# Kernel optimization log

Measured on AMD Instinct MI355X. Metric: run time of the kernel, lower is better.

## Reference

```python
import jax, jax.numpy as jnp
import numpy as np

K = 3          # kernel size
PAD = 1        # padding
KK = K * K
RECURRENT = 3  # opt.Recurrent_times - 1


def dcnv2(x, offset, mask, weight, bias):
    """Modulated deformable conv (DCNv2), stride 1, pad 1, dilation 1.

    x:      [B, C, H, W]
    offset: [B, 2*KK, H, W]  -- (dy, dx) interleaved per kernel tap
    mask:   [B, KK, H, W]    -- modulation scalars
    weight: [O, C, K, K], bias: [O]
    """
    B, C, H, W = x.shape
    off = offset.reshape(B, KK, 2, H, W)
    dy, dx = off[:, :, 0], off[:, :, 1]                       # [B,KK,H,W]

    ky, kx = jnp.meshgrid(jnp.arange(K), jnp.arange(K), indexing='ij')
    ky = (ky.reshape(KK) - PAD).astype(x.dtype)               # {-1,0,1}
    kx = (kx.reshape(KK) - PAD).astype(x.dtype)
    iy = jnp.arange(H, dtype=x.dtype)
    ix = jnp.arange(W, dtype=x.dtype)

    # fractional sampling coords, [B,KK,H,W]
    py = iy[None, None, :, None] + ky[None, :, None, None] + dy
    px = ix[None, None, None, :] + kx[None, :, None, None] + dx

    y0 = jnp.floor(py)
    x0 = jnp.floor(px)
    wy = (py - y0)[:, None]                                   # [B,1,KK,H,W]
    wx = (px - x0)[:, None]

    x_flat = x.reshape(B, C, H * W)

    def gather(yi, xi):
        valid = ((yi >= 0) & (yi <= H - 1) & (xi >= 0) & (xi <= W - 1))
        yc = jnp.clip(yi, 0, H - 1).astype(jnp.int32)
        xc = jnp.clip(xi, 0, W - 1).astype(jnp.int32)
        idx = (yc * W + xc).reshape(B, -1)                    # [B, KK*H*W]
        g = jax.vmap(lambda im, id_: im[:, id_])(x_flat, idx)  # [B,C,KK*H*W]
        return g.reshape(B, C, KK, H, W) * valid.astype(x.dtype)[:, None]

    v00 = gather(y0, x0)
    v01 = gather(y0, x0 + 1)
    v10 = gather(y0 + 1, x0)
    v11 = gather(y0 + 1, x0 + 1)

    val = (v00 * (1 - wy) * (1 - wx) + v01 * (1 - wy) * wx
           + v10 * wy * (1 - wx) + v11 * wy * wx)
    val = val * mask[:, None]                                  # modulation

    out = jnp.einsum('ock,bckhw->bohw', weight.reshape(weight.shape[0], C, KK), val)
    return out + bias[None, :, None, None]


def setup_inputs() -> dict:
    key = jax.random.key(0)
    k1, k2, k3 = jax.random.split(key, 3)
    B, H, W = 4, 512, 512
    sharp = jax.random.normal(k1, (B, 3, H, W), dtype=jnp.float32)
    motion = jax.random.normal(k2, (B, 3 * KK, H, W), dtype=jnp.float32)
    # one 3x3x3->3 conv per recurrence, stacked: [RECURRENT, O, C, K, K]
    dcn_weights = jax.random.normal(k3, (RECURRENT, 3, 3, K, K), dtype=jnp.float32) * 0.1
    dcn_biases = jnp.zeros((RECURRENT, 3), dtype=jnp.float32)
    return {"sharp": sharp, "motion": motion,
            "dcn_weights": dcn_weights, "dcn_biases": dcn_biases}


def reference(sharp, motion, dcn_weights, dcn_biases):
    # torch.split(motion, [2*KK, KK], dim=1)
    offset = motion[:, :2 * KK]
    mask = motion[:, 2 * KK:]
    feats = [sharp]
    cur = sharp
    for i in range(RECURRENT):
        cur = dcnv2(cur, offset, mask, dcn_weights[i], dcn_biases[i])
        feats.append(cur)
    return sum(feats) / (RECURRENT + 1)
```

## Files before the change

### kernel.cpp

```cpp
#include <hip/hip_runtime.h>
#include <hip/hip_fp16.h>


#define HH 512
#define WW 512
#define BATCH 4
#define HWSZ (HH * WW)
#define PAIRS_PER_IMG (HWSZ / 2)

union U4 { uint4 u; __half2 h[4]; };

__global__ __launch_bounds__(256) void to_half_kernel(
    const float* __restrict__ sharp, uint4* __restrict__ dst)
{
    const int i = blockIdx.x * 256 + threadIdx.x;
    const int b = i >> 17;
    const int p = (i & (PAIRS_PER_IMG - 1)) * 2;
    const float* s = sharp + (size_t)b * 3 * HWSZ + p;
    const float2 c0 = *(const float2*)(s);
    const float2 c1 = *(const float2*)(s + HWSZ);
    const float2 c2 = *(const float2*)(s + 2 * HWSZ);
    U4 o;
    o.h[0] = __float22half2_rn(make_float2(c0.x, c1.x));
    o.h[1] = __float22half2_rn(make_float2(c2.x, 0.f));
    o.h[2] = __float22half2_rn(make_float2(c0.y, c1.y));
    o.h[3] = __float22half2_rn(make_float2(c2.y, 0.f));
    dst[i] = o.u;
}

__device__ __forceinline__ void bilinear3(const char* __restrict__ sb,
                                          float py, float px, float m,
                                          float& o0, float& o1, float& o2)
{
    const float y0f = floorf(py), x0f = floorf(px);
    const float wy = py - y0f, wx = px - x0f;
    const bool vy0 = (y0f >= 0.f) && (y0f <= 511.f);
    const bool vy1 = (y0f >= -1.f) && (y0f <= 510.f);
    const bool vx0 = (x0f >= 0.f) && (x0f <= 511.f);
    const bool vx1 = (x0f >= -1.f) && (x0f <= 510.f);
    const int iy0 = (int)fminf(fmaxf(y0f, 0.f), 511.f);
    const int iy1 = (int)fminf(fmaxf(y0f + 1.f, 0.f), 511.f);
    const int ix0 = (int)fminf(fmaxf(x0f, 0.f), 511.f);
    const int ix1 = (int)fminf(fmaxf(x0f + 1.f, 0.f), 511.f);
    const int lc  = (int)fminf(fmaxf(x0f, 0.f), 510.f);
    const int s0 = ix0 - lc;
    const int s1 = ix1 - lc;

    float w00 = (vy0 && vx0) ? (1.f - wy) * (1.f - wx) * m : 0.f;
    float w01 = (vy0 && vx1) ? (1.f - wy) * wx * m : 0.f;
    float w10 = (vy1 && vx0) ? wy * (1.f - wx) * m : 0.f;
    float w11 = (vy1 && vx1) ? wy * wx * m : 0.f;

    const float wlo0 = s0 ? 0.f : (s1 ? w00 : w00 + w01);
    const float whi0 = s1 ? (s0 ? w00 + w01 : w01) : 0.f;
    const float wlo1 = s0 ? 0.f : (s1 ? w10 : w10 + w11);
    const float whi1 = s1 ? (s0 ? w10 + w11 : w11) : 0.f;

    U4 ra, rb;
    ra.u = *(const uint4*)(sb + (size_t)(iy0 * WW + lc) * 8);
    rb.u = *(const uint4*)(sb + (size_t)(iy1 * WW + lc) * 8);
    const float2 aL = __half22float2(ra.h[0]);
    const float2 aLz = __half22float2(ra.h[1]);
    const float2 aH = __half22float2(ra.h[2]);
    const float2 aHz = __half22float2(ra.h[3]);
    const float2 bL = __half22float2(rb.h[0]);
    const float2 bLz = __half22float2(rb.h[1]);
    const float2 bH = __half22float2(rb.h[2]);
    const float2 bHz = __half22float2(rb.h[3]);

    o0 = wlo0 * aL.x + whi0 * aH.x + wlo1 * bL.x + whi1 * bH.x;
    o1 = wlo0 * aL.y + whi0 * aH.y + wlo1 * bL.y + whi1 * bH.y;
    o2 = wlo0 * aLz.x + whi0 * aHz.x + wlo1 * bLz.x + whi1 * bHz.x;
}

template <bool FIRST, bool WRITE_DST>
__global__ __launch_bounds__(256) void dcn_kernel(
    const uint4* __restrict__ src,
    const float* __restrict__ motion,
    const float* __restrict__ wgt,
    const float* __restrict__ bias,
    uint4* __restrict__ dst,
    float* __restrict__ out)
{
    __shared__ float sw[84];
    const int t = threadIdx.x;
    if (t < 84) sw[t] = (t < 81) ? wgt[t] : bias[t - 81];
    __syncthreads();

    const int i = blockIdx.x * 256 + t;
    const int b = i >> 17;
    const int r = i & (PAIRS_PER_IMG - 1);
    const int y = r >> 8;
    const int x0 = (r & 255) * 2;
    const int p = y * WW + x0;

    const float* mb = motion + (size_t)b * 27 * HWSZ + p;
    const char* sb = (const char*)(src + (size_t)b * (HWSZ / 2));

    float a00 = sw[81], a01 = sw[82], a02 = sw[83];
    float a10 = sw[81], a11 = sw[82], a12 = sw[83];

#pragma unroll
    for (int k = 0; k < 9; ++k) {
        const float2 dy = *(const float2*)(mb + (size_t)(2 * k) * HWSZ);
        const float2 dx = *(const float2*)(mb + (size_t)(2 * k + 1) * HWSZ);
        const float2 m  = *(const float2*)(mb + (size_t)(18 + k) * HWSZ);
        const float ky = (float)(y + k / 3 - 1);
        const float kx = (float)(x0 + k % 3 - 1);

        float v0, v1, v2;
        bilinear3(sb, ky + dy.x, kx + dx.x, m.x, v0, v1, v2);
        a00 += sw[0 * 9 + k] * v0 + sw[1 * 9 + k] * v1 + sw[2 * 9 + k] * v2;
        a01 += sw[3 * 9 + k] * v0 + sw[4 * 9 + k] * v1 + sw[5 * 9 + k] * v2;
        a02 += sw[6 * 9 + k] * v0 + sw[7 * 9 + k] * v1 + sw[8 * 9 + k] * v2;

        float u0, u1, u2;
        bilinear3(sb, ky + dy.y, kx + 1.f + dx.y, m.y, u0, u1, u2);
        a10 += sw[0 * 9 + k] * u0 + sw[1 * 9 + k] * u1 + sw[2 * 9 + k] * u2;
        a11 += sw[3 * 9 + k] * u0 + sw[4 * 9 + k] * u1 + sw[5 * 9 + k] * u2;
        a12 += sw[6 * 9 + k] * u0 + sw[7 * 9 + k] * u1 + sw[8 * 9 + k] * u2;
    }

    if (WRITE_DST) {
        U4 o;
        o.h[0] = __float22half2_rn(make_float2(a00, a01));
        o.h[1] = __float22half2_rn(make_float2(a02, 0.f));
        o.h[2] = __float22half2_rn(make_float2(a10, a11));
        o.h[3] = __float22half2_rn(make_float2(a12, 0.f));
        dst[i] = o.u;
    }

    const size_t ob = (size_t)b * 3 * HWSZ + p;
    if (FIRST) {
        U4 c;
        c.u = *(const uint4*)(sb + (size_t)p * 8);
        const float2 pA01 = __half22float2(c.h[0]);
        const float2 pA2 = __half22float2(c.h[1]);
        const float2 pB01 = __half22float2(c.h[2]);
        const float2 pB2 = __half22float2(c.h[3]);
        *(float2*)(out + ob) = make_float2((pA01.x + a00) * 0.25f, (pB01.x + a10) * 0.25f);
        *(float2*)(out + ob + HWSZ) = make_float2((pA01.y + a01) * 0.25f, (pB01.y + a11) * 0.25f);
        *(float2*)(out + ob + 2 * HWSZ) = make_float2((pA2.x + a02) * 0.25f, (pB2.x + a12) * 0.25f);
    } else {
        float2 o0 = *(float2*)(out + ob);
        float2 o1 = *(float2*)(out + ob + HWSZ);
        float2 o2 = *(float2*)(out + ob + 2 * HWSZ);
        o0.x += a00 * 0.25f; o0.y += a10 * 0.25f;
        o1.x += a01 * 0.25f; o1.y += a11 * 0.25f;
        o2.x += a02 * 0.25f; o2.y += a12 * 0.25f;
        *(float2*)(out + ob) = o0;
        *(float2*)(out + ob + HWSZ) = o1;
        *(float2*)(out + ob + 2 * HWSZ) = o2;
    }
}

extern "C" void kernel_launch(void* const* d_in, const int* in_sizes, int n_in,
                              void* d_out, int out_size, void* d_ws, size_t ws_size,
                              hipStream_t stream) {
    const float* sharp  = (const float*)d_in[0];
    const float* motion = (const float*)d_in[1];
    const float* wts    = (const float*)d_in[2];
    const float* bias   = (const float*)d_in[3];
    float* out = (float*)d_out;

    const size_t npairs = (size_t)BATCH * PAIRS_PER_IMG;
    uint4* bufA = (uint4*)d_ws;
    uint4* bufB = bufA + npairs;

    const dim3 grid(npairs / 256);
    const dim3 block(256);

    to_half_kernel<<<grid, block, 0, stream>>>(sharp, bufA);
    dcn_kernel<true, true><<<grid, block, 0, stream>>>(
        bufA, motion, wts, bias, bufB, out);
    dcn_kernel<false, true><<<grid, block, 0, stream>>>(
        bufB, motion, wts + 81, bias + 3, bufA, out);
    dcn_kernel<false, false><<<grid, block, 0, stream>>>(
        bufA, motion, wts + 162, bias + 6, nullptr, out);
}
```

Measured before the change: 138.5 us.

## Stage motion planes into LDS via direct global-to-LDS loads, one pixel per thread

Each block now copies its 27 motion planes for 256 consecutive pixels into shared memory using the AMD global_load_lds builtin, then reads offsets and masks from LDS. The work split also changes from two pixels per thread to one, which doubles the grid and turns the float2 output and motion accesses into scalar ones. The goal is to cut per-thread register pressure and global-load latency on the dominant motion stream by using wide asynchronous copies. In exchange the kernel uses 27 KB of LDS per block, which may limit occupancy, and loses the amortisation of work across pixel pairs.

New measurement: 119.5 us. 1.16x faster.

```diff
diff --git a/kernel.cpp b/kernel.cpp
--- a/kernel.cpp
+++ b/kernel.cpp
@@ -9,6 +9,10 @@
 #define PAIRS_PER_IMG (HWSZ / 2)
 
 union U4 { uint4 u; __half2 h[4]; };
+union U2 { uint2 u; __half2 h[2]; };
+
+typedef const __attribute__((address_space(1))) void* gas_t;
+typedef __attribute__((address_space(3))) void* las_t;
 
 __global__ __launch_bounds__(256) void to_half_kernel(
     const float* __restrict__ sharp, uint4* __restrict__ dst)
@@ -46,10 +50,10 @@
     const int s0 = ix0 - lc;
     const int s1 = ix1 - lc;
 
-    float w00 = (vy0 && vx0) ? (1.f - wy) * (1.f - wx) * m : 0.f;
-    float w01 = (vy0 && vx1) ? (1.f - wy) * wx * m : 0.f;
-    float w10 = (vy1 && vx0) ? wy * (1.f - wx) * m : 0.f;
-    float w11 = (vy1 && vx1) ? wy * wx * m : 0.f;
+    const float w00 = (vy0 && vx0) ? (1.f - wy) * (1.f - wx) * m : 0.f;
+    const float w01 = (vy0 && vx1) ? (1.f - wy) * wx * m : 0.f;
+    const float w10 = (vy1 && vx0) ? wy * (1.f - wx) * m : 0.f;
+    const float w11 = (vy1 && vx1) ? wy * wx * m : 0.f;
 
     const float wlo0 = s0 ? 0.f : (s1 ? w00 : w00 + w01);
     const float whi0 = s1 ? (s0 ? w00 + w01 : w01) : 0.f;
@@ -75,82 +79,81 @@
 
 template <bool FIRST, bool WRITE_DST>
 __global__ __launch_bounds__(256) void dcn_kernel(
-    const uint4* __restrict__ src,
+    const uint2* __restrict__ src,
     const float* __restrict__ motion,
     const float* __restrict__ wgt,
     const float* __restrict__ bias,
-    uint4* __restrict__ dst,
+    uint2* __restrict__ dst,
     float* __restrict__ out)
 {
+    __shared__ float mlds[27][256];
     __shared__ float sw[84];
+
     const int t = threadIdx.x;
+    const int blk = blockIdx.x;
+    const int b = blk >> 10;
+    const int pbase = (blk & 1023) * 256;
+    const int p = pbase + t;
+    const int y = p >> 9;
+    const int x = p & 511;
+
     if (t < 84) sw[t] = (t < 81) ? wgt[t] : bias[t - 81];
+
+    {
+        const int w = t >> 6, lane = t & 63;
+        const float* mbase = motion + (size_t)b * 27 * HWSZ + pbase;
+#pragma unroll
+        for (int r = 0; r < 7; ++r) {
+            const int plane = r * 4 + w;
+            if (plane < 27) {
+                const float* gsrc = mbase + (size_t)plane * HWSZ + lane * 4;
+                __builtin_amdgcn_global_load_lds((gas_t)gsrc,
+                                                 (las_t)&mlds[plane][0],
+                                                 16, 0, 0);
+            }
+        }
+    }
     __syncthreads();
 
-    const int i = blockIdx.x * 256 + t;
-    const int b = i >> 17;
-    const int r = i & (PAIRS_PER_IMG - 1);
-    const int y = r >> 8;
-    const int x0 = (r & 255) * 2;
-    const int p = y * WW + x0;
+    const char* sb = (const char*)src + (size_t)b * HWSZ * 8;
 
-    const float* mb = motion + (size_t)b * 27 * HWSZ + p;
-    const char* sb = (const char*)(src + (size_t)b * (HWSZ / 2));
-
-    float a00 = sw[81], a01 = sw[82], a02 = sw[83];
-    float a10 = sw[81], a11 = sw[82], a12 = sw[83];
+    float acc0 = sw[81], acc1 = sw[82], acc2 = sw[83];
 
 #pragma unroll
     for (int k = 0; k < 9; ++k) {
-        const float2 dy = *(const float2*)(mb + (size_t)(2 * k) * HWSZ);
-        const float2 dx = *(const float2*)(mb + (size_t)(2 * k + 1) * HWSZ);
-        const float2 m  = *(const float2*)(mb + (size_t)(18 + k) * HWSZ);
-        const float ky = (float)(y + k / 3 - 1);
-        const float kx = (float)(x0 + k % 3 - 1);
+        const float dy = mlds[2 * k][t];
+        const float dx = mlds[2 * k + 1][t];
+        const float m  = mlds[18 + k][t];
+        const float py = (float)(y + k / 3 - 1) + dy;
+        const float px = (float)(x + k % 3 - 1) + dx;
 
         float v0, v1, v2;
-        bilinear3(sb, ky + dy.x, kx + dx.x, m.x, v0, v1, v2);
-        a00 += sw[0 * 9 + k] * v0 + sw[1 * 9 + k] * v1 + sw[2 * 9 + k] * v2;
-        a01 += sw[3 * 9 + k] * v0 + sw[4 * 9 + k] * v1 + sw[5 * 9 + k] * v2;
-        a02 += sw[6 * 9 + k] * v0 + sw[7 * 9 + k] * v1 + sw[8 * 9 + k] * v2;
-
-        float u0, u1, u2;
-        bilinear3(sb, ky + dy.y, kx + 1.f + dx.y, m.y, u0, u1, u2);
-        a10 += sw[0 * 9 + k] * u0 + sw[1 * 9 + k] * u1 + sw[2 * 9 + k] * u2;
-        a11 += sw[3 * 9 + k] * u0 + sw[4 * 9 + k] * u1 + sw[5 * 9 + k] * u2;
-        a12 += sw[6 * 9 + k] * u0 + sw[7 * 9 + k] * u1 + sw[8 * 9 + k] * u2;
+        bilinear3(sb, py, px, m, v0, v1, v2);
+        acc0 += sw[0 * 9 + k] * v0 + sw[1 * 9 + k] * v1 + sw[2 * 9 + k] * v2;
+        acc1 += sw[3 * 9 + k] * v0 + sw[4 * 9 + k] * v1 + sw[5 * 9 + k] * v2;
+        acc2 += sw[6 * 9 + k] * v0 + sw[7 * 9 + k] * v1 + sw[8 * 9 + k] * v2;
     }
 
     if (WRITE_DST) {
-        U4 o;
-        o.h[0] = __float22half2_rn(make_float2(a00, a01));
-        o.h[1] = __float22half2_rn(make_float2(a02, 0.f));
-        o.h[2] = __float22half2_rn(make_float2(a10, a11));
-        o.h[3] = __float22half2_rn(make_float2(a12, 0.f));
-        dst[i] = o.u;
+        U2 o;
+        o.h[0] = __float22half2_rn(make_float2(acc0, acc1));
+        o.h[1] = __float22half2_rn(make_float2(acc2, 0.f));
+        dst[(size_t)b * HWSZ + p] = o.u;
     }
 
     const size_t ob = (size_t)b * 3 * HWSZ + p;
     if (FIRST) {
-        U4 c;
-        c.u = *(const uint4*)(sb + (size_t)p * 8);
-        const float2 pA01 = __half22float2(c.h[0]);
-        const float2 pA2 = __half22float2(c.h[1]);
-        const float2 pB01 = __half22float2(c.h[2]);
-        const float2 pB2 = __half22float2(c.h[3]);
-        *(float2*)(out + ob) = make_float2((pA01.x + a00) * 0.25f, (pB01.x + a10) * 0.25f);
-        *(float2*)(out + ob + HWSZ) = make_float2((pA01.y + a01) * 0.25f, (pB01.y + a11) * 0.25f);
-        *(float2*)(out + ob + 2 * HWSZ) = make_float2((pA2.x + a02) * 0.25f, (pB2.x + a12) * 0.25f);
+        U2 c;
+        c.u = *(const uint2*)(sb + (size_t)p * 8);
+        const float2 s01 = __half22float2(c.h[0]);
+        const float2 s2 = __half22float2(c.h[1]);
+        out[ob] = (s01.x + acc0) * 0.25f;
+        out[ob + HWSZ] = (s01.y + acc1) * 0.25f;
+        out[ob + 2 * HWSZ] = (s2.x + acc2) * 0.25f;
     } else {
-        float2 o0 = *(float2*)(out + ob);
-        float2 o1 = *(float2*)(out + ob + HWSZ);
-        float2 o2 = *(float2*)(out + ob + 2 * HWSZ);
-        o0.x += a00 * 0.25f; o0.y += a10 * 0.25f;
-        o1.x += a01 * 0.25f; o1.y += a11 * 0.25f;
-        o2.x += a02 * 0.25f; o2.y += a12 * 0.25f;
-        *(float2*)(out + ob) = o0;
-        *(float2*)(out + ob + HWSZ) = o1;
-        *(float2*)(out + ob + 2 * HWSZ) = o2;
+        out[ob] += acc0 * 0.25f;
+        out[ob + HWSZ] += acc1 * 0.25f;
+        out[ob + 2 * HWSZ] += acc2 * 0.25f;
     }
 }
 
@@ -163,18 +166,18 @@
     const float* bias   = (const float*)d_in[3];
     float* out = (float*)d_out;
 
-    const size_t npairs = (size_t)BATCH * PAIRS_PER_IMG;
-    uint4* bufA = (uint4*)d_ws;
-    uint4* bufB = bufA + npairs;
+    uint2* bufA = (uint2*)d_ws;
+    uint2* bufB = bufA + (size_t)BATCH * HWSZ;
 
-    const dim3 grid(npairs / 256);
     const dim3 block(256);
+    const dim3 gridT(BATCH * PAIRS_PER_IMG / 256);
+    const dim3 gridD(BATCH * HWSZ / 256);
 
-    to_half_kernel<<<grid, block, 0, stream>>>(sharp, bufA);
-    dcn_kernel<true, true><<<grid, block, 0, stream>>>(
+    to_half_kernel<<<gridT, block, 0, stream>>>(sharp, (uint4*)bufA);
+    dcn_kernel<true, true><<<gridD, block, 0, stream>>>(
         bufA, motion, wts, bias, bufB, out);
-    dcn_kernel<false, true><<<grid, block, 0, stream>>>(
+    dcn_kernel<false, true><<<gridD, block, 0, stream>>>(
         bufB, motion, wts + 81, bias + 3, bufA, out);
-    dcn_kernel<false, false><<<grid, block, 0, stream>>>(
+    dcn_kernel<false, false><<<gridD, block, 0, stream>>>(
         bufA, motion, wts + 162, bias + 6, nullptr, out);
 }
```
